# Kernel tuning notes

Measured on AMD Instinct MI355X. Metric: run time of the kernel, lower is better.

Reference implementation:

```python
import jax, jax.numpy as jnp
import numpy as np

V = 50000      # tokenizer vocab size
E = 128        # embedding_dim
H = 160        # encoder_hidden_dim (bidirectional -> 2H)
D = 196        # decoder_hidden_dim
A = 224        # attention_dim
BN = 56        # bottle_neck_dim
PAD, START, END, UNK = 0, 1, 2, 3
COV_FACTOR = 0.75


def _lstm_step(x, h, c, Wi, Wh, bi, bh):
    # torch gate order: i, f, g, o
    g = x @ Wi.T + h @ Wh.T + bi + bh
    i, f, gg, o = jnp.split(g, 4, axis=-1)
    c = jax.nn.sigmoid(f) * c + jax.nn.sigmoid(i) * jnp.tanh(gg)
    h = jax.nn.sigmoid(o) * jnp.tanh(c)
    return h, c


def _run_lstm(x_tbe, Wi, Wh, bi, bh):
    B = x_tbe.shape[1]
    Hh = Wh.shape[1]
    def step(carry, xt):
        h, c = carry
        h, c = _lstm_step(xt, h, c, Wi, Wh, bi, bh)
        return (h, c), h
    init = (jnp.zeros((B, Hh), x_tbe.dtype), jnp.zeros((B, Hh), x_tbe.dtype))
    (hT, cT), hs = jax.lax.scan(step, init, x_tbe)
    return hs, hT, cT


def setup_inputs() -> dict:
    key = jax.random.key(0)
    ks = iter(jax.random.split(key, 48))
    def rn(shape, s=0.05):
        return jax.random.normal(next(ks), shape, jnp.float32) * s
    B, Tin, Ttgt = 32, 256, 100
    inp = {
        'batch_input_ids': jax.random.randint(next(ks), (B, Tin), 0, V + 50, dtype=jnp.int32),
        'batch_target_ids': jax.random.randint(next(ks), (B, Ttgt), 0, V + 50, dtype=jnp.int32),
        'max_num_oovs': 50,
        'emb': rn((V, E), 0.1),
        # bidirectional encoder LSTM
        'Wi_f': rn((4 * H, E)), 'Wh_f': rn((4 * H, H)),
        'bi_f': jnp.zeros(4 * H), 'bh_f': jnp.zeros(4 * H),
        'Wi_b': rn((4 * H, E)), 'Wh_b': rn((4 * H, H)),
        'bi_b': jnp.zeros(4 * H), 'bh_b': jnp.zeros(4 * H),
        # enc->dec bridges
        'Weh': rn((D, 2 * H)), 'beh': jnp.zeros(D),
        'Wec': rn((D, 2 * H)), 'bec': jnp.zeros(D),
        # decoder LSTMCell
        'Wi_d': rn((4 * D, E)), 'Wh_d': rn((4 * D, D)),
        'bi_d': jnp.zeros(4 * D), 'bh_d': jnp.zeros(4 * D),
        # attention
        'Wea': rn((A, 2 * H)), 'bea': jnp.zeros(A),
        'Wda': rn((A, D)),
        'Wca': rn((A, 1)),
        'v_attn': rn((1, A)),
        # vocab projection (bottleneck)
        'W1': rn((BN, D + 2 * H)), 'b1': jnp.zeros(BN),
        'W2': rn((V - END, BN)), 'b2': jnp.zeros(V - END),
        # p_gen switch
        'Wcs': rn((1, 2 * H)), 'bcs': jnp.zeros(1),
        'Wds': rn((1, D)),
        'Wes': rn((1, E)),
    }
    return inp


def reference(batch_input_ids, batch_target_ids, max_num_oovs, emb,
              Wi_f, Wh_f, bi_f, bh_f, Wi_b, Wh_b, bi_b, bh_b,
              Weh, beh, Wec, bec, Wi_d, Wh_d, bi_d, bh_d,
              Wea, bea, Wda, Wca, v_attn, W1, b1, W2, b2,
              Wcs, bcs, Wds, Wes):
    B, Tin = batch_input_ids.shape
    # map OOV input ids to <unk> for embedding lookup
    in_mapped = jnp.where(batch_input_ids >= V, UNK, batch_input_ids)
    x_tbe = emb[in_mapped].transpose(1, 0, 2)          # [Tin,B,E]
    hs_f, hTf, cTf = _run_lstm(x_tbe, Wi_f, Wh_f, bi_f, bh_f)
    hs_b, hTb, cTb = _run_lstm(x_tbe[::-1], Wi_b, Wh_b, bi_b, bh_b)
    enc = jnp.concatenate([hs_f, hs_b[::-1]], -1).transpose(1, 0, 2)  # [B,Tin,2H]
    h = jnp.concatenate([hTf, hTb], -1) @ Weh.T + beh   # [B,D]
    c = jnp.concatenate([cTf, cTb], -1) @ Wec.T + bec   # [B,D]
    enc_attn = enc @ Wea.T + bea                        # [B,Tin,A] (loop-invariant)
    pad_mask = batch_input_ids == PAD
    wca = Wca[:, 0]                                     # [A]
    cov0 = jnp.zeros((B, Tin))
    cur0 = jnp.full((B,), START, jnp.int32)

    def step(carry, nt):
        h, c, cov, cur, nll, cl = carry
        e = emb[cur]                                     # [B,E]
        h, c = _lstm_step(e, h, c, Wi_d, Wh_d, bi_d, bh_d)
        s = jnp.tanh(enc_attn + (h @ Wda.T)[:, None, :] + cov[:, :, None] * wca)
        s = s @ v_attn[0]                                # [B,Tin]
        s = jnp.where(pad_mask, -jnp.inf, s)
        attn = jax.nn.softmax(s, axis=1)                 # [B,Tin]
        ctx = jnp.einsum('bt,bth->bh', attn, enc)        # [B,2H]
        hc = jnp.concatenate([h, ctx], -1)
        vocab = jax.nn.softmax(jnp.tanh(hc @ W1.T + b1) @ W2.T + b2, axis=1)  # [B,V-END]
        p_gen = jax.nn.sigmoid(ctx @ Wcs[0] + bcs[0] + h @ Wds[0] + e @ Wes[0])  # [B]
        # F.pad(vocab, (END, max_num_oovs)).gather(1, nt): left-pad END zeros,
        # right-pad OOV zeros -> gen prob is vocab[nt-END] if END<=nt<V else 0
        idx = jnp.clip(nt - END, 0, vocab.shape[1] - 1)
        gen_p = jnp.take_along_axis(vocab, idx[:, None], axis=1)[:, 0]
        gen_p = jnp.where((nt >= END) & (nt < V), gen_p, 0.0)
        copy_p = jnp.sum(attn * (batch_input_ids == nt[:, None]), axis=1)
        p = p_gen * gen_p + (1.0 - p_gen) * copy_p
        nll = nll - jnp.log(p + 1e-9)
        cl = cl + jnp.minimum(attn, cov).sum(axis=1)
        cov = cov + attn
        cur = jnp.where(nt >= V, UNK, nt)
        return (h, c, cov, cur, nll, cl), None

    (h, c, cov, cur, nll, cl), _ = jax.lax.scan(
        step, (h, c, cov0, cur0, jnp.zeros(B), jnp.zeros(B)), batch_target_ids.T)
    nll_loss = nll.sum()
    cov_loss = cl.sum()
    return nll_loss, cov_loss, nll_loss + COV_FACTOR * cov_loss
```

## Files before the change

### kernel.cpp

```cpp
#include <hip/hip_runtime.h>

#define MSCOPE __HIP_MEMORY_SCOPE_AGENT

typedef __attribute__((ext_vector_type(8))) short bf16x8;
typedef __attribute__((ext_vector_type(4))) float f32x4;


constexpr size_t oXf   = 0;
constexpr size_t oXb   = oXf   + (size_t)8192*640;
constexpr size_t oXd   = oXb   + (size_t)8192*640;
constexpr size_t oHencB= oXd   + (size_t)3200*784;
constexpr size_t oEncA = oHencB+ (size_t)64*256*160;
constexpr size_t oEs   = oEncA + (size_t)8192*224;
constexpr size_t oCT   = oEs   + 3200;
constexpr size_t oH0   = oCT   + 10240;
constexpr size_t oC0   = oH0   + 6272;
constexpr size_t oHWdsAll = oC0 + 6272;
constexpr size_t oCtxWAll = oHWdsAll + 3200;
constexpr size_t oCopyAll = oCtxWAll + 3200;
constexpr size_t oZidxAll = oCopyAll + 3200;
constexpr size_t oClAll   = oZidxAll + 3200;
constexpr size_t oNllWg   = oClAll + 32;
constexpr size_t oW1cT    = oNllWg + 224;
constexpr size_t oAFl     = oW1cT + 17920;
constexpr size_t oAFa     = oAFl + 93184;
constexpr size_t oHdF     = oAFa + 32256;
constexpr size_t oFEnd    = oHdF + 358400;
constexpr size_t oUAll    = 0;
constexpr size_t oUPreAll = oUAll  + (size_t)100*1792;
constexpr size_t oHwdaAll = oUPreAll + (size_t)100*1792;
constexpr size_t oPartAll = oHwdaAll + (size_t)100*7168;
#define FENC(d,t,p)  ((((d)*256 + (t))*20 + (p))*16)
#define FLSTM(s,p)   (163840 + ((s)*8 + (p))*16)
#define FAUX(s,p)    (176640 + ((s)*8 + (p))*16)
#define FP2(s,m,b)   (189440 + (((s)*4 + (m))*32 + (b))*16)
#define CP3          394240
#define CFIN         394256
#define CENC         394272
constexpr int fEnd = 394288;
constexpr unsigned ENC_FULL  = 0xFFFFFu;

__device__ __forceinline__ float fast_tanh(float x){
  float e = __expf(-2.f*fabsf(x));
  float r = (1.f - e) * __builtin_amdgcn_rcpf(1.f + e);
  return copysignf(r, x);
}
__device__ __forceinline__ float sigm(float x){
  return __builtin_amdgcn_rcpf(1.f + __expf(-x));
}
__device__ __forceinline__ unsigned bfr(float f){
  unsigned u = __float_as_uint(f);
  return (u + 0x7FFFu + ((u>>16)&1u)) >> 16;
}
__device__ __forceinline__ float aload(const float* p){
  return __hip_atomic_load(const_cast<float*>(p), __ATOMIC_RELAXED, MSCOPE);
}
__device__ __forceinline__ float2 aload2(const float* p){
  unsigned long long u = __hip_atomic_load(
      reinterpret_cast<unsigned long long*>(const_cast<float*>(p)),
      __ATOMIC_RELAXED, MSCOPE);
  float2 r; __builtin_memcpy(&r, &u, 8); return r;
}
__device__ __forceinline__ void astore(float* p, float v){
  __hip_atomic_store(p, v, __ATOMIC_RELAXED, MSCOPE);
}
__device__ __forceinline__ void astoreu(unsigned* p, unsigned v){
  __hip_atomic_store(p, v, __ATOMIC_RELAXED, MSCOPE);
}
__device__ __forceinline__ void astore2(float* p, float a, float b){
  float2 t; t.x = a; t.y = b;
  unsigned long long u; __builtin_memcpy(&u, &t, 8);
  __hip_atomic_store(reinterpret_cast<unsigned long long*>(p), u,
                     __ATOMIC_RELAXED, MSCOPE);
}
__device__ __forceinline__ unsigned uload(unsigned* p){
  return __hip_atomic_load(p, __ATOMIC_RELAXED, MSCOPE);
}
__device__ __forceinline__ void set_line(unsigned* line){
  __hip_atomic_store(line, 1u, __ATOMIC_RELAXED, MSCOPE);
}
template<int SLP>
__device__ __forceinline__ void wait_lines(unsigned* base, int n, int tid){
  if (tid < 64){
    for(;;){
      bool miss = (tid < n) && (uload(base + tid*16) == 0u);
      if (__ballot(miss) == 0ULL) break;
      __builtin_amdgcn_s_sleep(SLP);
    }
  }
  __syncthreads();
}
__device__ __forceinline__ void add1(unsigned* word){
  (void)__hip_atomic_fetch_add(word, 1u, __ATOMIC_RELAXED, MSCOPE);
}
__device__ __forceinline__ float block_sum(float v, float* red){
  #pragma unroll
  for (int o=32;o;o>>=1) v += __shfl_down(v,o);
  if ((threadIdx.x&63)==0) red[threadIdx.x>>6] = v;
  __syncthreads();
  v = red[0]+red[1]+red[2]+red[3];
  __syncthreads();
  return v;
}

__global__ void prep_kernel(const int* __restrict__ in_ids, const int* __restrict__ tgt,
                            int* __restrict__ in_mapped, int* __restrict__ cur_ids,
                            unsigned* __restrict__ flags, float* __restrict__ hdF){
  const int g0 = blockIdx.x*256 + threadIdx.x, stride = gridDim.x*256;
  for (int i = g0; i < 8192; i += stride){
    int t = i >> 5, b = i & 31;
    int id = in_ids[b*256 + t];
    in_mapped[i] = (id >= 50000) ? 3 : id;
  }
  for (int i = g0; i < 3200; i += stride){
    int k = i >> 5, b = i & 31;
    int id = (k == 0) ? 1 : tgt[b*100 + (k-1)];
    cur_ids[i] = (id >= 50000) ? 3 : id;
  }
  for (int i = g0; i < fEnd; i += stride) flags[i] = 0u;
  for (int i = g0; i < 358400; i += stride) hdF[i] = 0.f;
}

struct RGArgs{ const int* gid; const float* emb; const float* W;
               const float* bias1; const float* bias2; float* out; int N; };
__global__ void __launch_bounds__(256) rowgemm(RGArgs a){
  __shared__ float rl[8*128];
  const int tid = threadIdx.x;
  const int N = a.N;
  const size_t r0 = (size_t)blockIdx.x*8;
  const size_t t = r0 >> 5; const int b0 = (int)(r0 & 31);
  for (int i = tid; i < 8*128; i += 256){
    int r = i >> 7, k = i & 127;
    rl[i] = a.emb[(size_t)a.gid[r0+r]*128 + k];
  }
  __syncthreads();
  for (int g = tid; g < N; g += 256){
    const float* wr = a.W + (size_t)g*128;
    float acc[8];
    #pragma unroll
    for (int r=0;r<8;r++) acc[r]=0.f;
    for (int k=0;k<128;k+=4){
      float4 wv = *(const float4*)(wr+k);
      #pragma unroll
      for (int r=0;r<8;r++){
        float4 xv = *(const float4*)(rl + r*128 + k);
        acc[r] += wv.x*xv.x + wv.y*xv.y + wv.z*xv.z + wv.w*xv.w;
      }
    }
    float bias = a.bias1[g] + a.bias2[g];
    float* op = a.out + ((size_t)t*N + g)*32 + b0;
    *(float4*)(op)   = make_float4(acc[0]+bias,acc[1]+bias,acc[2]+bias,acc[3]+bias);
    *(float4*)(op+4) = make_float4(acc[4]+bias,acc[5]+bias,acc[6]+bias,acc[7]+bias);
  }
}

struct MegaArgs{
  const float* Xf; const float* Xb; const float* Whf; const float* Whb;
  float* hencB; float* cT; unsigned* flg;
  const int* cur_ids; const float* emb;
  const float* Wi_d; const float* bi_d; const float* bh_d; float* Xd;
  const float* Whd; float* AFl;
  const float* Wda; const float* W1; const float* Wds; float* AFa;
  float* W1cT;
  const float* Wes; float* es;
};

__global__ void __launch_bounds__(256) enc_mega(MegaArgs a){
  extern __shared__ float sm[];
  const int blk = blockIdx.x, tid = threadIdx.x;

  if (blk < 40){
    float* Wl = sm;
    float* hl = sm + 5120;
    const int dir = blk/20, jwg = blk%20;
    const int b = tid & 31, jl = tid >> 5;
    const int j = jwg*8 + jl;
    const float* Wh = dir ? a.Whb : a.Whf;
    const float* X  = dir ? a.Xb  : a.Xf;
    float* HB = a.hencB + (size_t)dir*32*256*160;
    unsigned* flg = a.flg;
    for (int i = tid; i < 32*160; i += 256){
      int row = i/160, k = i - row*160;
      int gate = row >> 3, jj = row & 7;
      Wl[i] = Wh[((size_t)(gate*160 + jwg*8 + jj))*160 + k];
    }
    for (int i = tid; i < 32*164; i += 256) hl[i] = 0.f;
    float c = 0.f;
    const float4* w0 = (const float4*)(Wl + (0*8+jl)*160);
    const float4* w1 = (const float4*)(Wl + (1*8+jl)*160);
    const float4* w2 = (const float4*)(Wl + (2*8+jl)*160);
    const float4* w3 = (const float4*)(Wl + (3*8+jl)*160);
    __syncthreads();
    for (int t = 0; t < 256; ++t){
      const int trow = dir ? 255 - t : t;
      const float* xr = X + ((size_t)trow*640 + j)*32 + b;
      float g0 = xr[0], g1 = xr[5120], g2 = xr[10240], g3 = xr[15360];
      if (t > 0){
        wait_lines<2>(flg + FENC(dir, t-1, 0), 20, tid);
        const int tprev = dir ? (256 - t) : (t-1);
        for (int i2 = tid; i2 < 2560; i2 += 256){
          int bb = i2/80, kk = (i2 - bb*80)*2;
          float2 v = aload2(HB + ((size_t)bb*256 + tprev)*160 + kk);
          *(float2*)(hl + bb*164 + kk) = v;
        }
      }
      __syncthreads();
      const float4* hr = (const float4*)(hl + b*164);
      #pragma unroll 4
      for (int q = 0; q < 40; ++q){
        float4 hv = hr[q];
        float4 a0 = w0[q], a1 = w1[q], a2 = w2[q], a3 = w3[q];
        g0 += hv.x*a0.x + hv.y*a0.y + hv.z*a0.z + hv.w*a0.w;
        g1 += hv.x*a1.x + hv.y*a1.y + hv.z*a1.z + hv.w*a1.w;
        g2 += hv.x*a2.x + hv.y*a2.y + hv.z*a2.z + hv.w*a2.w;
        g3 += hv.x*a3.x + hv.y*a3.y + hv.z*a3.z + hv.w*a3.w;
      }
      float ig = sigm(g0), fg = sigm(g1), gc = fast_tanh(g2), og = sigm(g3);
      c = fg*c + ig*gc;
      float h = og * fast_tanh(c);
      astore(&HB[((size_t)b*256 + trow)*160 + j], h);
      __syncthreads();
      if (tid == 0) set_line(flg + FENC(dir, t, jwg));
    }
    a.cT[dir*5120 + b*160 + j] = c;
    return;
  }

  if (blk < 440){
    float* rl = sm;
    const size_t r0 = (size_t)(blk - 40)*8;
    const size_t t = r0 >> 5; const int b0 = (int)(r0 & 31);
    for (int i = tid; i < 8*128; i += 256){
      int r = i >> 7, k = i & 127;
      rl[i] = a.emb[(size_t)a.cur_ids[r0+r]*128 + k];
    }
    __syncthreads();
    for (int g = tid; g < 784; g += 256){
      const float* wr = a.Wi_d + (size_t)g*128;
      float acc[8];
      #pragma unroll
      for (int r=0;r<8;r++) acc[r]=0.f;
      for (int k=0;k<128;k+=4){
        float4 wv = *(const float4*)(wr+k);
        #pragma unroll
        for (int r=0;r<8;r++){
          float4 xv = *(const float4*)(rl + r*128 + k);
          acc[r] += wv.x*xv.x + wv.y*xv.y + wv.z*xv.z + wv.w*xv.w;
        }
      }
      float bias = a.bi_d[g] + a.bh_d[g];
      float* op = a.Xd + ((size_t)t*784 + g)*32 + b0;
      *(float4*)(op)   = make_float4(acc[0]+bias,acc[1]+bias,acc[2]+bias,acc[3]+bias);
      *(float4*)(op+4) = make_float4(acc[4]+bias,acc[5]+bias,acc[6]+bias,acc[7]+bias);
    }
    return;
  }

  if (blk < 804){
    int dw = (blk - 440)*256 + tid;
    if (dw < 93184){
      int frag = dw>>2, d = dw&3;
      int T = frag/448, r2 = frag - T*448;
      int k7 = r2>>6, l = r2&63;
      int jb = T>>2, gate = T&3;
      int j = jb*16 + (l&15);
      int k0 = k7*32 + ((l>>4)<<3) + 2*d;
      unsigned lo=0, hi=0;
      if (j < 196){
        if (k0   < 196) lo = bfr(a.Whd[(size_t)(gate*196+j)*196 + k0]);
        if (k0+1 < 196) hi = bfr(a.Whd[(size_t)(gate*196+j)*196 + k0+1]);
      }
      ((unsigned*)a.AFl)[dw] = lo | (hi<<16);
    }
    if (dw < 32256){
      int frag = dw>>2, d = dw&3;
      int T = frag/448, r2 = frag - T*448;
      int k7 = r2>>6, l = r2&63;
      int ar = T*16 + (l&15);
      int k0 = k7*32 + ((l>>4)<<3) + 2*d;
      unsigned lo=0, hi=0;
      #pragma unroll
      for (int h = 0; h < 2; ++h){
        int k = k0 + h;
        float v = 0.f;
        if (k < 196){
          if (ar < 224) v = a.Wda[(size_t)ar*196 + k];
          else { int g = ar - 224;
            if (g < 56) v = a.W1[(size_t)g*516 + k];
            else if (g == 56) v = a.Wds[k];
          }
        }
        if (h == 0) lo = bfr(v); else hi = bfr(v);
      }
      ((unsigned*)a.AFa)[dw] = lo | (hi<<16);
    }
    return;
  }

  if (blk < 874){
    int i = (blk - 804)*256 + tid;
    if (i < 17920){ int q = i / 56, g = i - q*56; a.W1cT[q*56+g] = a.W1[(size_t)g*516 + 196 + q]; }
    return;
  }

  {
    int r = (blk - 874)*4 + (tid >> 6);
    int l = tid & 63;
    if (r < 3200){
      const float* e = a.emb + (size_t)a.cur_ids[r]*128;
      float acc = e[l]*a.Wes[l] + e[l+64]*a.Wes[l+64];
      #pragma unroll
      for (int o=32;o;o>>=1) acc += __shfl_down(acc,o);
      if (l==0) a.es[r] = acc;
    }
  }
}

__global__ void mid_kernel(const float* __restrict__ hencB, const float* __restrict__ cT,
                           const float* __restrict__ Weh, const float* __restrict__ beh,
                           const float* __restrict__ Wec, const float* __restrict__ bec,
                           float* __restrict__ h0, float* __restrict__ c0){
  __shared__ float hc[320], cc[320];
  int b = blockIdx.x, tid = threadIdx.x;
  if (tid < 160){
    hc[tid]     = hencB[((size_t)b*256 + 255)*160 + tid];
    hc[160+tid] = hencB[((size_t)(32+b)*256 + 0)*160 + tid];
    cc[tid]     = cT[b*160 + tid];
    cc[160+tid] = cT[5120 + b*160 + tid];
  }
  __syncthreads();
  for (int g = tid; g < 196; g += 256){
    const float* w1 = Weh + (size_t)g*320;
    const float* w2 = Wec + (size_t)g*320;
    float a1 = beh[g], a2 = bec[g];
    for (int k = 0; k < 320; ++k){ a1 += hc[k]*w1[k]; a2 += cc[k]*w2[k]; }
    h0[b*196 + g] = a1;
    c0[b*196 + g] = a2;
  }
}

struct DecArgs{
  const float* Xd; const float* hencB; float* encA;
  const float* h0; const float* c0; const float* AFl; const float* AFa;
  float* hdF;
  const float* Wea; const float* bea;
  const float* Wca; const float* vat; const float* W1cT; const float* b1;
  const float* W2; const float* b2;
  const float* Wcs; const float* bcs; const float* es;
  const int* in_ids; const int* tgt;
  float* uAll; float* uPreAll; float* hwdaAll;
  float* hWdsAll; float* ctxWAll; float* copyAll;
  float* zidxAll; float* partAll; float* clAll; float* nllWg; float* out;
  unsigned* flg;
};

__global__ void __launch_bounds__(256) dec_scan(DecArgs A){
  extern __shared__ float sm[];
  const int wg = blockIdx.x, tid = threadIdx.x;
  unsigned* flg = A.flg;

  if (wg < 8){
    const int q = wg;
    const int nUq  = (q < 5) ? 2 : 1;
    const int jb0q = q;
    const int jb1q = (q < 5) ? q + 8 : 0;
    const int auxB = (q < 5) ? q : (q == 5 ? 5 : (q == 6 ? 9 : 13));
    const int auxC = (q < 5) ? 1 : (q == 7 ? 5 : 4);
    unsigned* ldsu = (unsigned*)sm;
    bf16x8*   ldsf = (bf16x8*)sm;
    const int AB = nUq*1792;
    const int l = tid & 63, wv = tid >> 6;
    const int lq = l >> 4, lc = l & 15;
    const int u = wv >> 1, nt = wv & 1;
    const bool act = u < nUq;
    const int jb = (u == 0) ? jb0q : jb1q;
    {
      const unsigned* aflu = (const unsigned*)A.AFl;
      const unsigned* afau = (const unsigned*)A.AFa;
      const int totDw = (AB + auxC*448)*4;
      for (int i = tid; i < totDw; i += 256){
        int slot = i>>2, d = i&3;
        unsigned v;
        if (slot < AB){
          int uu = slot/1792, r = slot - uu*1792;
          int fi = r>>6, ll = r&63;
          int jbu = (uu == 0) ? jb0q : jb1q;
          int T = jbu*4 + fi/7, k7 = fi%7;
          v = aflu[(((size_t)T*7 + k7)*64 + ll)*4 + d];
        } else {
          int r = slot - AB;
          int a = r/448, r2 = r - a*448;
          int k7 = r2>>6, ll = r2&63;
          v = afau[((((size_t)(auxB + a))*7 + k7)*64 + ll)*4 + d];
        }
        ldsu[i] = v;
      }
    }
    float cst[4];
    if (act){
      int b = nt*16 + lc;
      #pragma unroll
      for (int i = 0; i < 4; ++i){
        int j = jb*16 + lq*4 + i;
        cst[i] = (j < 196) ? A.c0[b*196 + j] : 0.f;
      }
    }
    bf16x8 Bfr[7][2];
    #pragma unroll
    for (int k7 = 0; k7 < 7; ++k7)
      #pragma unroll
      for (int ntt = 0; ntt < 2; ++ntt){
        short tmp[8];
        #pragma unroll
        for (int e = 0; e < 8; ++e){
          int k = k7*32 + lq*8 + e;
          int b = ntt*16 + lc;
          float hv = (k < 196) ? A.h0[b*196 + k] : 0.f;
          tmp[e] = (short)bfr(hv);
        }
        __builtin_memcpy(&Bfr[k7][ntt], tmp, 16);
      }
    __syncthreads();
    unsigned* hdF = (unsigned*)A.hdF;
    for (int s = 0; s < 100; ++s){
      const float* Xs = A.Xd + (size_t)s*25088;
      if (act){
        float xg4[4][4];
        #pragma unroll
        for (int g = 0; g < 4; ++g)
          #pragma unroll
          for (int i = 0; i < 4; ++i){
            int j = jb*16 + lq*4 + i;
            int b = nt*16 + lc;
            xg4[g][i] = (j < 196) ? Xs[((size_t)(g*196 + j))*32 + b] : 0.f;
          }
        f32x4 acc[4];
        #pragma unroll
        for (int g = 0; g < 4; ++g){
          f32x4 a0 = {0.f,0.f,0.f,0.f};
          #pragma unroll
          for (int k7 = 0; k7 < 7; ++k7){
            bf16x8 af = ldsf[(u*28 + g*7 + k7)*64 + l];
            a0 = __builtin_amdgcn_mfma_f32_16x16x32_bf16(af, Bfr[k7][nt], a0, 0,0,0);
          }
          acc[g] = a0;
        }
        float hv4[4];
        #pragma unroll
        for (int i = 0; i < 4; ++i){
          float I = acc[0][i]+xg4[0][i], F = acc[1][i]+xg4[1][i];
          float G = acc[2][i]+xg4[2][i], O = acc[3][i]+xg4[3][i];
          float cc = sigm(F)*cst[i] + sigm(I)*fast_tanh(G);
          cst[i] = cc;
          hv4[i] = sigm(O)*fast_tanh(cc);
        }
        #pragma unroll
        for (int p = 0; p < 2; ++p){
          int jp = jb*16 + lq*4 + 2*p;
          if (jp < 196){
            int k7 = jp>>5, tl = lc | (((jp>>3)&3)<<4), d = (jp&7)>>1;
            unsigned w = bfr(hv4[2*p]) | (bfr(hv4[2*p+1])<<16);
            astoreu(&hdF[(size_t)s*3584 + ((k7*2+nt)*64 + tl)*4 + d], w);
          }
        }
      }
      __syncthreads();
      if (tid == 0) set_line(flg + FLSTM(s, q));
      wait_lines<1>(flg + FLSTM(s, 0), 8, tid);
      {
        const float* hp = (const float*)(hdF + (size_t)s*3584);
        #pragma unroll
        for (int k7 = 0; k7 < 7; ++k7)
          #pragma unroll
          for (int ntt = 0; ntt < 2; ++ntt){
            float2 v0 = aload2(hp + (((k7*2+ntt)*64 + l)*4));
            float2 v1 = aload2(hp + (((k7*2+ntt)*64 + l)*4 + 2));
            unsigned dwv[4];
            __builtin_memcpy(dwv, &v0, 8); __builtin_memcpy(dwv+2, &v1, 8);
            __builtin_memcpy(&Bfr[k7][ntt], dwv, 16);
          }
      }
      for (int a = wv; a < auxC; a += 4){
        int T = auxB + a;
        #pragma unroll
        for (int ntt = 0; ntt < 2; ++ntt){
          f32x4 acc = {0.f,0.f,0.f,0.f};
          #pragma unroll
          for (int k7 = 0; k7 < 7; ++k7){
            bf16x8 af = ldsf[AB + (a*7 + k7)*64 + l];
            acc = __builtin_amdgcn_mfma_f32_16x16x32_bf16(af, Bfr[k7][ntt], acc, 0,0,0);
          }
          int b = ntt*16 + lc;
          #pragma unroll
          for (int p = 0; p < 2; ++p){
            int ar = T*16 + lq*4 + 2*p;
            float v0 = acc[2*p], v1 = acc[2*p+1];
            if (ar < 224){
              astore2(&A.hwdaAll[(size_t)s*7168 + b*224 + ar], v0, v1);
            } else {
              int g = ar - 224;
              if (g < 56) astore2(&A.uPreAll[(size_t)s*1792 + b*56 + g], v0, v1);
              else if (g == 56) astore(&A.hWdsAll[s*32 + b], v0);
            }
          }
        }
      }
      __syncthreads();
      if (tid == 0) set_line(flg + FAUX(s, q));
    }
    return;
  }

  if (wg < 40){
    const int b = wg - 8;
    float* hwdaL = sm;
    float* attnL = sm + 224;
    float* pctx  = sm + 480;
    float* ctxL  = sm + 1440;
    float* red   = sm + 1760;
    float* pu    = sm + 1764;
    float* wcaL  = sm + 1988;
    float* vL    = sm + 2212;
    float* WcsL  = sm + 2436;
    float* b1L   = sm + 2756;
    if (tid < 224){ wcaL[tid] = A.Wca[tid]; vL[tid] = A.vat[tid]; }
    for (int i = tid; i < 320; i += 256) WcsL[i] = A.Wcs[i];
    if (tid < 56) b1L[tid] = A.b1[tid];
    const int inid = A.in_ids[b*256 + tid];
    const float4* erow = (const float4*)(A.encA + (size_t)(b*256 + tid)*224);
    float cov = 0.f, clr = 0.f;
    if (tid == 0){
      while (uload(flg + CENC) != 216u) __builtin_amdgcn_s_sleep(8);
    }
    __syncthreads();
    for (int s = 0; s < 100; ++s){
      wait_lines<2>(flg + FAUX(s, 0), 8, tid);
      if (tid < 224) hwdaL[tid] = aload(&A.hwdaAll[(size_t)s*7168 + b*224 + tid]);
      __syncthreads();
      float exv = 0.f;
      if (inid != 0){
        float acc = 0.f;
        #pragma unroll 8
        for (int q = 0; q < 56; ++q){
          float4 ev = erow[q]; int a0 = 4*q;
          acc += fast_tanh(ev.x + hwdaL[a0]   + cov*wcaL[a0]  )*vL[a0];
          acc += fast_tanh(ev.y + hwdaL[a0+1] + cov*wcaL[a0+1])*vL[a0+1];
          acc += fast_tanh(ev.z + hwdaL[a0+2] + cov*wcaL[a0+2])*vL[a0+2];
          acc += fast_tanh(ev.w + hwdaL[a0+3] + cov*wcaL[a0+3])*vL[a0+3];
        }
        exv = __expf(acc);
      }
      float S = block_sum(exv, red);
      float attn = exv * __builtin_amdgcn_rcpf(S);
      attnL[tid] = attn;
      const int ntb = A.tgt[b*100 + s];
      float cpS = block_sum((inid == ntb) ? attn : 0.f, red);
      float mnS = block_sum(fminf(attn, cov), red);
      if (tid == 0){
        astore(&A.copyAll[s*32 + b], cpS);
        clr += mnS;
        if (s == 99) astore(&A.clAll[b], clr);
      }
      cov += attn;
      if (tid < 240){
        int seg = tid/80, h4i = tid - seg*80;
        int t0 = seg*86, t1 = (t0+86 < 256) ? t0+86 : 256;
        const float* base = (h4i < 40)
          ? (A.hencB + ((size_t)b*256)*160 + (size_t)h4i*4)
          : (A.hencB + ((size_t)(32+b)*256)*160 + (size_t)(h4i-40)*4);
        float4 accv = {0.f,0.f,0.f,0.f};
        #pragma unroll 4
        for (int t2 = t0; t2 < t1; ++t2){
          float av = attnL[t2];
          float4 ev = *(const float4*)(base + (size_t)t2*160);
          accv.x += av*ev.x; accv.y += av*ev.y; accv.z += av*ev.z; accv.w += av*ev.w;
        }
        *(float4*)(pctx + (seg*80+h4i)*4) = accv;
      }
      __syncthreads();
      if (tid < 80){
        float4 p0 = *(float4*)(pctx + tid*4);
        float4 p1 = *(float4*)(pctx + (80+tid)*4);
        float4 p2v = *(float4*)(pctx + (160+tid)*4);
        float4 cvv;
        cvv.x = p0.x+p1.x+p2v.x; cvv.y = p0.y+p1.y+p2v.y;
        cvv.z = p0.z+p1.z+p2v.z; cvv.w = p0.w+p1.w+p2v.w;
        *(float4*)(ctxL + tid*4) = cvv;
      }
      __syncthreads();
      if (tid < 224){
        int g = tid % 56, seg = tid / 56;
        float acc = 0.f;
        const float* wp = A.W1cT + (size_t)seg*80*56 + g;
        #pragma unroll 4
        for (int q = 0; q < 80; ++q) acc += ctxL[seg*80 + q] * wp[q*56];
        pu[seg*56 + g] = acc;
      } else {
        int l = tid - 224; float acc = 0.f;
        for (int q = l; q < 320; q += 32) acc += ctxL[q]*WcsL[q];
        #pragma unroll
        for (int o=16;o;o>>=1) acc += __shfl_down(acc,o,32);
        if (l==0) astore(&A.ctxWAll[s*32 + b], acc);
      }
      __syncthreads();
      if (tid < 56){
        float upre = aload(&A.uPreAll[(size_t)s*1792 + b*56 + tid]);
        float uu = fast_tanh(upre + b1L[tid] + pu[tid] + pu[56+tid] + pu[112+tid] + pu[168+tid]);
        astore(&A.uAll[(size_t)s*1792 + b*56 + tid], uu);
      }
      __syncthreads();
      if (tid == 0){
        set_line(flg + FP2(s,0,b));
        set_line(flg + FP2(s,1,b));
        set_line(flg + FP2(s,2,b));
        set_line(flg + FP2(s,3,b));
      }
    }
    return;
  }

  {
    const int wgv = wg - 40;
    {
      float* hlrow = sm;
      for (int rr = 0; rr < 38; ++rr){
        int row = wgv*38 + rr;
        if (row < 8192){
          int b = row >> 8, t = row & 255;
          for (int k = tid; k < 320; k += 256)
            hlrow[k] = (k < 160) ? A.hencB[((size_t)b*256 + t)*160 + k]
                                 : A.hencB[((size_t)(32+b)*256 + t)*160 + (k-160)];
          __syncthreads();
          if (tid < 224){
            const float* wr = A.Wea + (size_t)tid*320;
            float acc = A.bea[tid];
            for (int k = 0; k < 320; k += 4){
              float4 wv = *(const float4*)(wr+k);
              float4 xv = *(const float4*)(hlrow+k);
              acc += wv.x*xv.x + wv.y*xv.y + wv.z*xv.z + wv.w*xv.w;
            }
            astore(&A.encA[(size_t)row*224 + tid], acc);
          }
          __syncthreads();
        }
      }
      __syncthreads();
      if (tid == 0) add1(flg + CENC);
    }
    const int vs = (int)(((long long)wgv*49998)/216);
    const int ve = (int)(((long long)(wgv+1)*49998)/216);
    const int v = vs + tid;
    const bool valid = v < ve;
    const int vc = valid ? v : 0;
    float4 w2r[14];
    {
      const float4* wr = (const float4*)(A.W2 + (size_t)vc*56);
      #pragma unroll
      for (int q=0;q<14;++q) w2r[q] = wr[q];
    }
    const float b2v = A.b2[vc];
    float* ulL  = sm;
    float* redW = sm + 1792;
    int*   idxL = (int*)(sm + 1920);
    float* red  = sm + 1952;
    const int lane = tid & 63, wv2 = tid >> 6;
    for (int s = 0; s < 100; ++s){
      int nt3 = (tid < 32) ? A.tgt[tid*100 + s] : 0;
      wait_lines<8>(flg + FP2(s, wgv & 3, 0), 32, tid);
      for (int i2 = tid; i2 < 896; i2 += 256){
        float2 u2 = aload2(&A.uAll[(size_t)s*1792 + i2*2]);
        *(float2*)(ulL + i2*2) = u2;
      }
      if (tid < 32){
        int ix = nt3 - 2; ix = ix<0?0:(ix>49997?49997:ix);
        idxL[tid] = ix;
      }
      __syncthreads();
      #pragma unroll 4
      for (int bb=0; bb<32; ++bb){
        const float4* uv = (const float4*)(ulL + bb*56);
        float z = b2v;
        #pragma unroll
        for (int q=0;q<14;++q){
          float4 u4 = uv[q];
          z += w2r[q].x*u4.x + w2r[q].y*u4.y + w2r[q].z*u4.z + w2r[q].w*u4.w;
        }
        if (valid && v == idxL[bb]) astore(&A.zidxAll[s*32+bb], z);
        float sv2 = valid ? __expf(z) : 0.f;
        #pragma unroll
        for (int o=32;o;o>>=1) sv2 += __shfl_down(sv2,o);
        if (lane == 0) redW[wv2*32+bb] = sv2;
      }
      __syncthreads();
      if (tid < 32){
        float tot = redW[tid]+redW[32+tid]+redW[64+tid]+redW[96+tid];
        astore(&A.partAll[(size_t)(s*32+tid)*216 + wgv], tot);
      }
      __syncthreads();
    }
    __syncthreads();
    if (tid == 0) add1(flg + CP3);
    if (tid == 0){
      while (uload(flg + CP3) != 216u) __builtin_amdgcn_s_sleep(32);
    }
    __syncthreads();
    float nll1 = 0.f;
    for (int p = wgv; p < 3200; p += 216){
      float pv = (tid < 216) ? aload(&A.partAll[(size_t)p*216 + tid]) : 0.f;
      float se = block_sum(pv, red);
      if (tid == 0){
        int s = p >> 5, b = p & 31;
        int nt2 = A.tgt[b*100 + s];
        float xg = aload(&A.ctxWAll[p]) + A.bcs[0] + aload(&A.hWdsAll[p]) + A.es[p];
        float pg = 1.f/(1.f + __expf(-xg));
        float genp = (nt2 >= 2 && nt2 < 50000) ? (__expf(aload(&A.zidxAll[p])) / se) : 0.f;
        float pr = pg*genp + (1.f-pg)*aload(&A.copyAll[p]);
        nll1 += -logf(pr + 1e-9f);
      }
    }
    if (tid == 0) astore(&A.nllWg[wgv], nll1);
    __syncthreads();
    if (tid == 0) add1(flg + CFIN);
    if (wg == 40){
      if (tid == 0){
        while (uload(flg + CFIN) != 216u) __builtin_amdgcn_s_sleep(32);
      }
      __syncthreads();
      float nv = (tid < 216) ? aload(&A.nllWg[tid]) : 0.f;
      float nll = block_sum(nv, red);
      float cv = (tid < 32) ? aload(&A.clAll[tid]) : 0.f;
      float cl = block_sum(cv, red);
      if (tid == 0){ A.out[0]=nll; A.out[1]=cl; A.out[2]=nll + 0.75f*cl; }
    }
  }
}

extern "C" void kernel_launch(void* const* d_in, const int* in_sizes, int n_in,
                              void* d_out, int out_size, void* d_ws, size_t ws_size,
                              hipStream_t stream){
  const int*   in_ids = (const int*)  d_in[0];
  const int*   tgt    = (const int*)  d_in[1];
  const float* emb    = (const float*)d_in[3];
  const float* Wi_f   = (const float*)d_in[4];
  const float* Wh_f   = (const float*)d_in[5];
  const float* bi_f   = (const float*)d_in[6];
  const float* bh_f   = (const float*)d_in[7];
  const float* Wi_b   = (const float*)d_in[8];
  const float* Wh_b   = (const float*)d_in[9];
  const float* bi_b   = (const float*)d_in[10];
  const float* bh_b   = (const float*)d_in[11];
  const float* Weh    = (const float*)d_in[12];
  const float* beh    = (const float*)d_in[13];
  const float* Wec    = (const float*)d_in[14];
  const float* bec    = (const float*)d_in[15];
  const float* Wi_d   = (const float*)d_in[16];
  const float* Wh_d   = (const float*)d_in[17];
  const float* bi_d   = (const float*)d_in[18];
  const float* bh_d   = (const float*)d_in[19];
  const float* Wea    = (const float*)d_in[20];
  const float* bea    = (const float*)d_in[21];
  const float* Wda    = (const float*)d_in[22];
  const float* Wca    = (const float*)d_in[23];
  const float* vat    = (const float*)d_in[24];
  const float* W1     = (const float*)d_in[25];
  const float* b1     = (const float*)d_in[26];
  const float* W2     = (const float*)d_in[27];
  const float* b2     = (const float*)d_in[28];
  const float* Wcs    = (const float*)d_in[29];
  const float* bcs    = (const float*)d_in[30];
  const float* Wds    = (const float*)d_in[31];
  const float* Wes    = (const float*)d_in[32];

  float* ws = (float*)d_ws;
  int* iBase = (int*)(ws + oFEnd);
  int* in_mapped = iBase;
  int* cur_ids   = iBase + 8192;
  unsigned* flags = (unsigned*)(iBase + 11392);

  prep_kernel<<<512, 256, 0, stream>>>(in_ids, tgt, in_mapped, cur_ids, flags,
                                       ws + oHdF);

  { RGArgs a{in_mapped, emb, Wi_f, bi_f, bh_f, ws + oXf, 640};
    rowgemm<<<1024, 256, 0, stream>>>(a); }
  { RGArgs a{in_mapped, emb, Wi_b, bi_b, bh_b, ws + oXb, 640};
    rowgemm<<<1024, 256, 0, stream>>>(a); }

  { MegaArgs ma{ws + oXf, ws + oXb, Wh_f, Wh_b, ws + oHencB, ws + oCT, flags,
                cur_ids, emb, Wi_d, bi_d, bh_d, ws + oXd,
                Wh_d, ws + oAFl, Wda, W1, Wds, ws + oAFa,
                ws + oW1cT, Wes, ws + oEs};
    enc_mega<<<dim3(1674), dim3(256), (5120 + 32*164)*4, stream>>>(ma); }

  mid_kernel<<<32, 256, 0, stream>>>(ws + oHencB, ws + oCT, Weh, beh, Wec, bec,
                                     ws + oH0, ws + oC0);

  { DecArgs da{ws + oXd, ws + oHencB, ws + oEncA,
               ws + oH0, ws + oC0, ws + oAFl, ws + oAFa,
               ws + oHdF,
               Wea, bea,
               Wca, vat, ws + oW1cT, b1, W2, b2, Wcs, bcs, ws + oEs,
               in_ids, tgt,
               ws + oUAll, ws + oUPreAll, ws + oHwdaAll,
               ws + oHWdsAll, ws + oCtxWAll, ws + oCopyAll,
               ws + oZidxAll, ws + oPartAll, ws + oClAll, ws + oNllWg, (float*)d_out,
               flags};
    dec_scan<<<dim3(256), dim3(256), 64512, stream>>>(da); }
}
```

Measured before the change: 4.866 ms.

## Move encoder attention projection out of decoder scan into separate tiled GEMM kernel

Computes encA (the encoder-side attention projection) in a new standalone kernel that processes 8 rows per block and reuses each Wea row load across those 8 rows. Previously the vocab workgroups inside the persistent decoder kernel did this work one row at a time, and the attention workgroups spun on a completion counter before starting. Removing that in-kernel dependency and flag means the decoder starts with encA already finished. The cost is an extra kernel launch on the critical path, and the overlap with decoder startup that the fused version allowed is lost.

```diff
diff --git a/kernel.cpp b/kernel.cpp
--- a/kernel.cpp
+++ b/kernel.cpp
@@ -36,8 +36,7 @@
 #define FP2(s,m,b)   (189440 + (((s)*4 + (m))*32 + (b))*16)
 #define CP3          394240
 #define CFIN         394256
-#define CENC         394272
-constexpr int fEnd = 394288;
+constexpr int fEnd = 394272;
 constexpr unsigned ENC_FULL  = 0xFFFFFu;
 
 __device__ __forceinline__ float fast_tanh(float x){
@@ -339,11 +338,42 @@
   }
 }
 
+__global__ void __launch_bounds__(256) encA_gemm(const float* __restrict__ hencB,
+                 const float* __restrict__ Wea, const float* __restrict__ bea,
+                 float* __restrict__ encA){
+  __shared__ float rl[8*320];
+  const int tid = threadIdx.x;
+  const size_t r0 = (size_t)blockIdx.x*8;
+  for (int i = tid; i < 8*320; i += 256){
+    int r = i/320, k = i - r*320;
+    size_t row = r0 + r; int b = (int)(row >> 8), t = (int)(row & 255);
+    rl[i] = (k < 160) ? hencB[((size_t)b*256 + t)*160 + k]
+                      : hencB[((size_t)(32+b)*256 + t)*160 + (k-160)];
+  }
+  __syncthreads();
+  for (int g = tid; g < 224; g += 256){
+    const float* wr = Wea + (size_t)g*320;
+    float acc[8];
+    #pragma unroll
+    for (int r=0;r<8;r++) acc[r]=0.f;
+    for (int k=0;k<320;k+=4){
+      float4 wv = *(const float4*)(wr+k);
+      #pragma unroll
+      for (int r=0;r<8;r++){
+        float4 xv = *(const float4*)(rl + r*320 + k);
+        acc[r] += wv.x*xv.x + wv.y*xv.y + wv.z*xv.z + wv.w*xv.w;
+      }
+    }
+    float bias = bea[g];
+    #pragma unroll
+    for (int r=0;r<8;r++) encA[(r0+r)*224 + g] = acc[r] + bias;
+  }
+}
+
 struct DecArgs{
-  const float* Xd; const float* hencB; float* encA;
+  const float* Xd; const float* hencB; const float* encA;
   const float* h0; const float* c0; const float* AFl; const float* AFa;
   float* hdF;
-  const float* Wea; const float* bea;
   const float* Wca; const float* vat; const float* W1cT; const float* b1;
   const float* W2; const float* b2;
   const float* Wcs; const float* bcs; const float* es;
@@ -529,9 +559,6 @@
     const int inid = A.in_ids[b*256 + tid];
     const float4* erow = (const float4*)(A.encA + (size_t)(b*256 + tid)*224);
     float cov = 0.f, clr = 0.f;
-    if (tid == 0){
-      while (uload(flg + CENC) != 216u) __builtin_amdgcn_s_sleep(8);
-    }
     __syncthreads();
     for (int s = 0; s < 100; ++s){
       wait_lines<2>(flg + FAUX(s, 0), 8, tid);
@@ -621,32 +648,6 @@
 
   {
     const int wgv = wg - 40;
-    {
-      float* hlrow = sm;
-      for (int rr = 0; rr < 38; ++rr){
-        int row = wgv*38 + rr;
-        if (row < 8192){
-          int b = row >> 8, t = row & 255;
-          for (int k = tid; k < 320; k += 256)
-            hlrow[k] = (k < 160) ? A.hencB[((size_t)b*256 + t)*160 + k]
-                                 : A.hencB[((size_t)(32+b)*256 + t)*160 + (k-160)];
-          __syncthreads();
-          if (tid < 224){
-            const float* wr = A.Wea + (size_t)tid*320;
-            float acc = A.bea[tid];
-            for (int k = 0; k < 320; k += 4){
-              float4 wv = *(const float4*)(wr+k);
-              float4 xv = *(const float4*)(hlrow+k);
-              acc += wv.x*xv.x + wv.y*xv.y + wv.z*xv.z + wv.w*xv.w;
-            }
-            astore(&A.encA[(size_t)row*224 + tid], acc);
-          }
-          __syncthreads();
-        }
-      }
-      __syncthreads();
-      if (tid == 0) add1(flg + CENC);
-    }
     const int vs = (int)(((long long)wgv*49998)/216);
     const int ve = (int)(((long long)(wgv+1)*49998)/216);
     const int v = vs + tid;
@@ -794,10 +795,11 @@
   mid_kernel<<<32, 256, 0, stream>>>(ws + oHencB, ws + oCT, Weh, beh, Wec, bec,
                                      ws + oH0, ws + oC0);
 
+  encA_gemm<<<1024, 256, 0, stream>>>(ws + oHencB, Wea, bea, ws + oEncA);
+
   { DecArgs da{ws + oXd, ws + oHencB, ws + oEncA,
                ws + oH0, ws + oC0, ws + oAFl, ws + oAFa,
                ws + oHdF,
-               Wea, bea,
                Wca, vat, ws + oW1cT, b1, W2, b2, Wcs, bcs, ws + oEs,
                in_ids, tgt,
                ws + oUAll, ws + oUPreAll, ws + oHwdaAll,
```

Result: faster. 4.565 ms (-6.2%).
